# Kernel optimization log

Hardware: AMD Instinct MI355X
Metric: run time of the kernel (lower is better)

## Reference

```python
import jax, jax.numpy as jnp
import numpy as np

D = 1024      # embed_dim
H = 16        # num_heads
HD = D // H   # head_dim


def setup_inputs() -> dict:
    key = jax.random.key(0)
    ks = jax.random.split(key, 9)
    s = 0.02
    x = jax.random.normal(ks[0], (8, 1024, D), dtype=jnp.float32)
    # Per-head Q/K/V linears, torch Linear layout [out, in] -> stacked [H, HD, D]
    Wq = jax.random.normal(ks[1], (H, HD, D), dtype=jnp.float32) * s
    Wk = jax.random.normal(ks[2], (H, HD, D), dtype=jnp.float32) * s
    Wv = jax.random.normal(ks[3], (H, HD, D), dtype=jnp.float32) * s
    bq = jax.random.normal(ks[4], (H, HD), dtype=jnp.float32) * s
    bk = jax.random.normal(ks[5], (H, HD), dtype=jnp.float32) * s
    bv = jax.random.normal(ks[6], (H, HD), dtype=jnp.float32) * s
    Wo = jax.random.normal(ks[7], (D, D), dtype=jnp.float32) * s
    bo = jax.random.normal(ks[8], (D,), dtype=jnp.float32) * s
    return {"x": x, "Wq": Wq, "Wk": Wk, "Wv": Wv,
            "bq": bq, "bk": bk, "bv": bv, "Wo": Wo, "bo": bo}


def reference(x, Wq, Wk, Wv, bq, bk, bv, Wo, bo):
    # Batched per-head projections: [B,S,D] x [H,HD,D] -> [B,H,S,HD]
    q = jnp.einsum('bsd,hkd->bhsk', x, Wq) + bq[None, :, None, :]
    k = jnp.einsum('bsd,hkd->bhsk', x, Wk) + bk[None, :, None, :]
    v = jnp.einsum('bsd,hkd->bhsk', x, Wv) + bv[None, :, None, :]
    scores = jnp.einsum('bhqk,bhsk->bhqs', q, k) / jnp.sqrt(jnp.float32(HD))
    probs = jax.nn.softmax(scores, axis=-1)          # [B,H,S,S]
    attn = jnp.einsum('bhqs,bhsk->bhqk', probs, v)   # [B,H,S,HD]
    # Concat heads along feature dim -> [B,S,D]
    B, _, S, _ = attn.shape
    concat = jnp.transpose(attn, (0, 2, 1, 3)).reshape(B, S, D)
    out = jnp.einsum('bsd,ed->bse', concat, Wo) + bo  # output projection
    return out
```

## Files before the change

kernel.cpp:

```cpp
#include <hip/hip_runtime.h>
#include <stdint.h>
#include <stddef.h>


typedef short bf16x8 __attribute__((ext_vector_type(8)));
typedef float f32x4  __attribute__((ext_vector_type(4)));
typedef unsigned short u16x8 __attribute__((ext_vector_type(8)));
typedef unsigned short u16x4 __attribute__((ext_vector_type(4)));

#define MFMA16 __builtin_amdgcn_mfma_f32_16x16x32_bf16

typedef const void __attribute__((address_space(1)))* gas1_t;
typedef void __attribute__((address_space(3)))* las3_t;

static __device__ __forceinline__ void gload16(const void* g, void* l) {
  __builtin_amdgcn_global_load_lds((gas1_t)g, (las3_t)l, 16, 0, 0);
}

static __device__ __forceinline__ unsigned short f2bf(float f) {
  union { float f; unsigned int u; } v; v.f = f;
  unsigned int r = v.u + 0x7fffu + ((v.u >> 16) & 1u);
  return (unsigned short)(r >> 16);
}

__global__ __launch_bounds__(256) void cast_all(
    const float* __restrict__ x, const float* __restrict__ Wq,
    const float* __restrict__ Wk, const float* __restrict__ Wv,
    const float* __restrict__ Wo,
    unsigned short* __restrict__ xb, unsigned short* __restrict__ wqkv,
    unsigned short* __restrict__ wob) {
  int base = (blockIdx.x * 256 + threadIdx.x) * 4;
  const float* s; unsigned short* d;
  if (base < 8388608) { s = x + base; d = xb + base; }
  else if (base < 11534336) {
    int o = base - 8388608; int wi = o >> 20;
    const float* w = (wi == 0) ? Wq : (wi == 1) ? Wk : Wv;
    s = w + (o & 1048575); d = wqkv + o;
  } else {
    int o = base - 11534336; s = Wo + o; d = wob + o;
  }
  float4 f = *(const float4*)s;
  u16x4 r; r[0] = f2bf(f.x); r[1] = f2bf(f.y); r[2] = f2bf(f.z); r[3] = f2bf(f.w);
  *(u16x4*)d = r;
}

__global__ __launch_bounds__(512, 2) void gemm256_qkv(
    const unsigned short* __restrict__ Ag, const unsigned short* __restrict__ Bg,
    unsigned short* __restrict__ Qo, unsigned short* __restrict__ Ko,
    unsigned short* __restrict__ Vo,
    const float* __restrict__ bq, const float* __restrict__ bk,
    const float* __restrict__ bv) {
  __shared__ __align__(16) char sm[131072];
  const int tid = threadIdx.x, lane = tid & 63, w = tid >> 6;
  const int wr = w >> 2, wc = w & 3;
  const int l15 = lane & 15, g = lane >> 4;
  const int bcol = blockIdx.x * 256, brow = blockIdx.y * 256;

  auto stage2 = [&](int kt, int buf, int p) {
#pragma unroll
    for (int jj = 0; jj < 2; ++jj) {
      int rowBase, region;
      const unsigned short* src;
      if (p < 2) {
        int j = p * 2 + jj;
        rowBase = wr * 128 + wc * 32 + j * 8;
        region = 0; src = Ag + (size_t)(brow + rowBase) * 1024;
      } else {
        int j = (p - 2) * 2 + jj;
        rowBase = (wc >> 1) * 128 + (wr * 2 + (wc & 1)) * 32 + j * 8;
        region = 32768; src = Bg + (size_t)(bcol + rowBase) * 1024;
      }
      int rlo = lane >> 3;
      int cl = (lane & 7) ^ ((rowBase + rlo) & 7);
      gload16(src + (size_t)rlo * 1024 + kt * 64 + cl * 8,
              sm + buf * 65536 + region + rowBase * 128);
    }
  };

#pragma unroll
  for (int p = 0; p < 4; ++p) stage2(0, 0, p);
  asm volatile("s_waitcnt vmcnt(0)" ::: "memory");
  __builtin_amdgcn_s_barrier();

  f32x4 acc[8][4] = {};
  bf16x8 bfr[4];
  for (int t = 0; t < 16; ++t) {
    const int cur = t & 1;
    const char* As = sm + cur * 65536;
    const char* Bs = As + 32768;
#pragma unroll
    for (int ph = 0; ph < 4; ++ph) {
      const int qm = ph & 1, kk = ph >> 1;
      if (qm == 0) {
#pragma unroll
        for (int nc = 0; nc < 4; ++nc) {
          int row = wc * 64 + nc * 16 + l15;
          int off = (row * 128 + kk * 64 + g * 16) ^ ((row & 7) << 4);
          bfr[nc] = *(const bf16x8*)(Bs + off);
        }
      }
      bf16x8 af[4];
#pragma unroll
      for (int mr = 0; mr < 4; ++mr) {
        int row = wr * 128 + qm * 64 + mr * 16 + l15;
        int off = (row * 128 + kk * 64 + g * 16) ^ ((row & 7) << 4);
        af[mr] = *(const bf16x8*)(As + off);
      }
      if (t < 15) stage2(t + 1, cur ^ 1, ph);
      __builtin_amdgcn_s_barrier();
      __builtin_amdgcn_s_setprio(1);
#pragma unroll
      for (int mr = 0; mr < 4; ++mr)
#pragma unroll
        for (int nc = 0; nc < 4; ++nc)
          acc[qm * 4 + mr][nc] = MFMA16(af[mr], bfr[nc], acc[qm * 4 + mr][nc], 0, 0, 0);
      __builtin_amdgcn_s_setprio(0);
      if (ph == 3)
        asm volatile("s_waitcnt vmcnt(0)" ::: "memory");
      __builtin_amdgcn_s_barrier();
    }
  }

  const int bb_ = brow >> 10;
#pragma unroll
  for (int nc = 0; nc < 4; ++nc) {
    int n = bcol + wc * 64 + nc * 16 + l15;
    int tt = n >> 10, nh = n & 1023;
    int h = nh >> 6, hd = nh & 63;
    const float* bias = (tt == 0) ? bq : (tt == 1) ? bk : bv;
    float bbv = bias[nh];
    if (tt == 2) {
      size_t vtb = ((size_t)(bb_ * 16 + h) * 64 + hd) * 1024;
#pragma unroll
      for (int qm = 0; qm < 2; ++qm)
#pragma unroll
        for (int mr = 0; mr < 4; ++mr) {
          int m0 = brow + wr * 128 + qm * 64 + mr * 16 + g * 4;
          int srow0 = m0 & 1023;
          u16x4 vv;
#pragma unroll
          for (int r = 0; r < 4; ++r) vv[r] = f2bf(acc[qm * 4 + mr][nc][r] + bbv);
          *(u16x4*)(Vo + vtb + srow0) = vv;
        }
    } else {
      float scale = (tt == 0) ? 0.125f : 1.0f;
      unsigned short* dst = (tt == 0) ? Qo : Ko;
      size_t basei = ((size_t)(bb_ * 16 + h) * 1024) * 64 + hd;
#pragma unroll
      for (int qm = 0; qm < 2; ++qm)
#pragma unroll
        for (int mr = 0; mr < 4; ++mr)
#pragma unroll
          for (int r = 0; r < 4; ++r) {
            int m = brow + wr * 128 + qm * 64 + mr * 16 + g * 4 + r;
            dst[basei + (size_t)(m & 1023) * 64] = f2bf((acc[qm * 4 + mr][nc][r] + bbv) * scale);
          }
    }
  }
}

__global__ __launch_bounds__(256) void gemm128_out(
    const unsigned short* __restrict__ A, const unsigned short* __restrict__ Bm,
    float* __restrict__ Cf, const float* __restrict__ bO) {
  __shared__ __align__(16) char sm[65536];
  const int tid = threadIdx.x, lane = tid & 63, w = tid >> 6;
  const int wr = w >> 1, wc = w & 1;
  const int bcol = (blockIdx.x & 7) * 128, brow = (blockIdx.x >> 3) * 128;
  const int l15 = lane & 15, g = lane >> 4;

  auto stage = [&](int ks, int buf) {
    char* Ad = sm + buf * 32768;
    char* Bd = Ad + 16384;
#pragma unroll
    for (int jj = 0; jj < 4; ++jj) {
      int p = (w * 4 + jj) * 1024 + lane * 16;
      int row = p >> 7;
      int cl = (lane & 7) ^ (row & 7);
      gload16(A + (size_t)(brow + row) * 1024 + ks * 64 + cl * 8,
              Ad + (w * 4 + jj) * 1024);
      gload16(Bm + (size_t)(bcol + row) * 1024 + ks * 64 + cl * 8,
              Bd + (w * 4 + jj) * 1024);
    }
  };

  stage(0, 0);
  asm volatile("s_waitcnt vmcnt(0)" ::: "memory");
  __syncthreads();

  f32x4 acc[4][4] = {};
  for (int ks = 0; ks < 16; ++ks) {
    const int cur = ks & 1;
    if (ks < 15) stage(ks + 1, cur ^ 1);
    const char* As = sm + cur * 32768;
    const char* Bs = As + 16384;
#pragma unroll
    for (int kk = 0; kk < 2; ++kk) {
      bf16x8 af[4], bfr[4];
#pragma unroll
      for (int mi = 0; mi < 4; ++mi) {
        int row = wr * 64 + mi * 16 + l15;
        int off = (row * 128 + kk * 64 + g * 16) ^ ((row & 7) << 4);
        af[mi] = *(const bf16x8*)(As + off);
      }
#pragma unroll
      for (int ni = 0; ni < 4; ++ni) {
        int row = wc * 64 + ni * 16 + l15;
        int off = (row * 128 + kk * 64 + g * 16) ^ ((row & 7) << 4);
        bfr[ni] = *(const bf16x8*)(Bs + off);
      }
#pragma unroll
      for (int mi = 0; mi < 4; ++mi)
#pragma unroll
        for (int ni = 0; ni < 4; ++ni)
          acc[mi][ni] = MFMA16(af[mi], bfr[ni], acc[mi][ni], 0, 0, 0);
    }
    asm volatile("s_waitcnt vmcnt(0)" ::: "memory");
    __syncthreads();
  }
#pragma unroll
  for (int ni = 0; ni < 4; ++ni) {
    int n = bcol + wc * 64 + ni * 16 + l15;
    float bb = bO[n];
#pragma unroll
    for (int mi = 0; mi < 4; ++mi)
#pragma unroll
      for (int r = 0; r < 4; ++r) {
        int m = brow + wr * 64 + mi * 16 + g * 4 + r;
        Cf[(size_t)m * 1024 + n] = acc[mi][ni][r] + bb;
      }
  }
}

__global__ __launch_bounds__(256, 3) void attn_fused(
    const unsigned short* __restrict__ Qb, const unsigned short* __restrict__ Kb,
    const unsigned short* __restrict__ VtG, unsigned short* __restrict__ Cc) {
  __shared__ __align__(16) char sm[49152];
  char* Ks = sm;
  char* Vt = sm + 16384;
  const int tid = threadIdx.x, lane = tid & 63, w = tid >> 6;
  char* Ps = sm + 32768 + w * 4096;
  const int l15 = lane & 15, g = lane >> 4;
  const int id = blockIdx.x;
  const int qt = id >> 7, bh = id & 127;
  const size_t hb = (size_t)bh * (1024 * 64);

  bf16x8 qreg[2][2];
#pragma unroll
  for (int kk = 0; kk < 2; ++kk)
#pragma unroll
    for (int ni = 0; ni < 2; ++ni) {
      int q = qt * 128 + w * 32 + ni * 16 + l15;
      qreg[kk][ni] = *(const bf16x8*)(Qb + hb + (size_t)q * 64 + kk * 32 + g * 8);
    }

  auto stage = [&](int c, int buf) {
#pragma unroll
    for (int j = 0; j < 2; ++j) {
      int p = (w * 2 + j) * 1024 + lane * 16;
      int row = p >> 7;
      int cl = (lane & 7) ^ (row & 7);
      gload16(Kb + hb + (size_t)(c * 64 + row) * 64 + cl * 8,
              Ks + buf * 8192 + (w * 2 + j) * 1024);
      gload16(VtG + hb + (size_t)row * 1024 + c * 64 + cl * 8,
              Vt + buf * 8192 + (w * 2 + j) * 1024);
    }
  };

  stage(0, 0);
  asm volatile("s_waitcnt vmcnt(0)" ::: "memory");
  __syncthreads();

  f32x4 acc[4][2] = {};
  float m_run[2] = {-1e30f, -1e30f};
  float l_run[2] = {0.f, 0.f};

  for (int c = 0; c < 16; ++c) {
    const int cur = c & 1;
    if (c < 15) stage(c + 1, cur ^ 1);
    const char* Kc = Ks + cur * 8192;
    const char* Vc = Vt + cur * 8192;

    f32x4 st[4][2] = {};
#pragma unroll
    for (int kk = 0; kk < 2; ++kk) {
      bf16x8 ka[4];
#pragma unroll
      for (int mi = 0; mi < 4; ++mi) {
        int row = mi * 16 + l15;
        int off = (row * 128 + kk * 64 + g * 16) ^ ((row & 7) << 4);
        ka[mi] = *(const bf16x8*)(Kc + off);
      }
#pragma unroll
      for (int mi = 0; mi < 4; ++mi)
#pragma unroll
        for (int ni = 0; ni < 2; ++ni)
          st[mi][ni] = MFMA16(ka[mi], qreg[kk][ni], st[mi][ni], 0, 0, 0);
    }

    float corr_s[2];
#pragma unroll
    for (int ni = 0; ni < 2; ++ni) {
      float mx = -1e30f;
#pragma unroll
      for (int mi = 0; mi < 4; ++mi)
#pragma unroll
        for (int r = 0; r < 4; ++r) mx = fmaxf(mx, st[mi][ni][r]);
      mx = fmaxf(mx, __shfl_xor(mx, 16));
      mx = fmaxf(mx, __shfl_xor(mx, 32));
      float mn = fmaxf(m_run[ni], mx);
      float corr = __expf(m_run[ni] - mn);
      float sum = 0.f;
      const int q = ni * 16 + l15;
      const int rbase = q * 128, sw = (q & 7) << 4;
#pragma unroll
      for (int mi = 0; mi < 4; ++mi) {
        u16x4 pk;
#pragma unroll
        for (int r = 0; r < 4; ++r) {
          float e = __expf(st[mi][ni][r] - mn);
          sum += e;
          pk[r] = f2bf(e);
        }
        *(u16x4*)(Ps + ((rbase + (mi * 16 + g * 4) * 2) ^ sw)) = pk;
      }
      sum += __shfl_xor(sum, 16);
      sum += __shfl_xor(sum, 32);
      l_run[ni] = l_run[ni] * corr + sum;
      m_run[ni] = mn;
      corr_s[ni] = corr;
    }

#pragma unroll
    for (int nd = 0; nd < 4; ++nd)
#pragma unroll
      for (int ni = 0; ni < 2; ++ni)
#pragma unroll
        for (int r = 0; r < 4; ++r)
          acc[nd][ni][r] *= corr_s[ni];

#pragma unroll
    for (int kk = 0; kk < 2; ++kk) {
      bf16x8 vf[4], pa[2];
#pragma unroll
      for (int nd = 0; nd < 4; ++nd) {
        int row = nd * 16 + l15;
        int off = (row * 128 + kk * 64 + g * 16) ^ ((row & 7) << 4);
        vf[nd] = *(const bf16x8*)(Vc + off);
      }
#pragma unroll
      for (int ni = 0; ni < 2; ++ni) {
        int q = ni * 16 + l15;
        int off = (q * 128 + kk * 64 + g * 16) ^ ((q & 7) << 4);
        pa[ni] = *(const bf16x8*)(Ps + off);
      }
#pragma unroll
      for (int nd = 0; nd < 4; ++nd)
#pragma unroll
        for (int ni = 0; ni < 2; ++ni)
          acc[nd][ni] = MFMA16(vf[nd], pa[ni], acc[nd][ni], 0, 0, 0);
    }

    asm volatile("s_waitcnt vmcnt(0)" ::: "memory");
    __syncthreads();
  }

  const int b = bh >> 4, h = bh & 15;
  float invl[2] = {1.f / l_run[0], 1.f / l_run[1]};
#pragma unroll
  for (int ni = 0; ni < 2; ++ni) {
    int q = qt * 128 + w * 32 + ni * 16 + l15;
    size_t rowb = (size_t)(b * 1024 + q) * 1024 + h * 64;
#pragma unroll
    for (int nd = 0; nd < 4; ++nd) {
      u16x4 o;
#pragma unroll
      for (int r = 0; r < 4; ++r) o[r] = f2bf(acc[nd][ni][r] * invl[ni]);
      *(u16x4*)(Cc + rowb + nd * 16 + g * 4) = o;
    }
  }
}

extern "C" void kernel_launch(void* const* d_in, const int* in_sizes, int n_in,
                              void* d_out, int out_size, void* d_ws, size_t ws_size,
                              hipStream_t stream) {
  const float* x  = (const float*)d_in[0];
  const float* Wq = (const float*)d_in[1];
  const float* Wk = (const float*)d_in[2];
  const float* Wv = (const float*)d_in[3];
  const float* bq = (const float*)d_in[4];
  const float* bk = (const float*)d_in[5];
  const float* bv = (const float*)d_in[6];
  const float* Wo = (const float*)d_in[7];
  const float* bo = (const float*)d_in[8];

  char* ws = (char*)d_ws;
  unsigned short* xb   = (unsigned short*)(ws);
  unsigned short* wqkv = (unsigned short*)(ws + 16777216);
  unsigned short* wob  = (unsigned short*)(ws + 23068672);
  unsigned short* Qb   = (unsigned short*)(ws + 25165824);
  unsigned short* Kb   = (unsigned short*)(ws + 41943040);
  unsigned short* VtG  = (unsigned short*)(ws + 58720256);
  unsigned short* Cc   = xb;

  cast_all<<<dim3(12288), dim3(256), 0, stream>>>(x, Wq, Wk, Wv, Wo, xb, wqkv, wob);
  gemm256_qkv<<<dim3(12, 32), dim3(512), 0, stream>>>(
      xb, wqkv, Qb, Kb, VtG, bq, bk, bv);
  attn_fused<<<dim3(1024), dim3(256), 0, stream>>>(Qb, Kb, VtG, Cc);
  gemm128_out<<<dim3(512), dim3(256), 0, stream>>>(Cc, wob, (float*)d_out, bo);
}
```

Baseline: 261.7 us.

## Deepen QKV GEMM pipeline to three in-flight half-K stages with new swizzle

The QKV projection GEMM now splits each 64-wide K tile into two 32-wide halves stored in separate LDS sub-buffers. Loads are issued three halves ahead, using counted vmcnt waits instead of draining to zero every tile. The LDS layout changes to 64-byte rows with a rotate-style swizzle, and B fragments are reloaded once per half. This is meant to hide global-load latency better, at the cost of more barriers per tile and finer-grained, more error-prone wait accounting.

```diff
diff --git a/kernel.cpp b/kernel.cpp
--- a/kernel.cpp
+++ b/kernel.cpp
@@ -56,67 +56,79 @@
   const int l15 = lane & 15, g = lane >> 4;
   const int bcol = blockIdx.x * 256, brow = blockIdx.y * 256;
 
-  auto stage2 = [&](int kt, int buf, int p) {
+  const int srow = (lane >> 2);
+  const int sc = lane & 3;
+  auto stageA = [&](int hh) {
+    char* Ad = sm + ((hh >> 1) & 1) * 65536 + (hh & 1) * 16384;
 #pragma unroll
     for (int jj = 0; jj < 2; ++jj) {
-      int rowBase, region;
-      const unsigned short* src;
-      if (p < 2) {
-        int j = p * 2 + jj;
-        rowBase = wr * 128 + wc * 32 + j * 8;
-        region = 0; src = Ag + (size_t)(brow + rowBase) * 1024;
-      } else {
-        int j = (p - 2) * 2 + jj;
-        rowBase = (wc >> 1) * 128 + (wr * 2 + (wc & 1)) * 32 + j * 8;
-        region = 32768; src = Bg + (size_t)(bcol + rowBase) * 1024;
-      }
-      int rlo = lane >> 3;
-      int cl = (lane & 7) ^ ((rowBase + rlo) & 7);
-      gload16(src + (size_t)rlo * 1024 + kt * 64 + cl * 8,
-              sm + buf * 65536 + region + rowBase * 128);
+      int r0 = (w * 2 + jj) * 16;
+      int r = r0 + srow;
+      int gph = (sc - (r >> 1)) & 3;
+      gload16(Ag + (size_t)(brow + r) * 1024 + hh * 32 + gph * 8, Ad + r0 * 64);
     }
   };
-
-#pragma unroll
-  for (int p = 0; p < 4; ++p) stage2(0, 0, p);
-  asm volatile("s_waitcnt vmcnt(0)" ::: "memory");
+  auto stageB = [&](int hh) {
+    char* Bd = sm + ((hh >> 1) & 1) * 65536 + 32768 + (hh & 1) * 16384;
+#pragma unroll
+    for (int jj = 0; jj < 2; ++jj) {
+      int r0 = (w * 2 + jj) * 16;
+      int r = r0 + srow;
+      int gph = (sc - (r >> 1)) & 3;
+      gload16(Bg + (size_t)(bcol + r) * 1024 + hh * 32 + gph * 8, Bd + r0 * 64);
+    }
+  };
+
+  stageA(0); stageB(0); stageA(1); stageB(1); stageA(2); stageB(2);
+  asm volatile("s_waitcnt vmcnt(8)" ::: "memory");
   __builtin_amdgcn_s_barrier();
 
   f32x4 acc[8][4] = {};
-  bf16x8 bfr[4];
   for (int t = 0; t < 16; ++t) {
-    const int cur = t & 1;
-    const char* As = sm + cur * 65536;
-    const char* Bs = As + 32768;
-#pragma unroll
-    for (int ph = 0; ph < 4; ++ph) {
-      const int qm = ph & 1, kk = ph >> 1;
-      if (qm == 0) {
-#pragma unroll
-        for (int nc = 0; nc < 4; ++nc) {
-          int row = wc * 64 + nc * 16 + l15;
-          int off = (row * 128 + kk * 64 + g * 16) ^ ((row & 7) << 4);
-          bfr[nc] = *(const bf16x8*)(Bs + off);
-        }
-      }
-      bf16x8 af[4];
+    const char* Tb = sm + (t & 1) * 65536;
+#pragma unroll
+    for (int kk = 0; kk < 2; ++kk) {
+      const int h = t * 2 + kk;
+      const char* Ab = Tb + kk * 16384;
+      const char* Bb = Tb + 32768 + kk * 16384;
+      bf16x8 bfr[4], af[4];
+#pragma unroll
+      for (int nc = 0; nc < 4; ++nc) {
+        int nr = wc * 64 + nc * 16 + l15;
+        bfr[nc] = *(const bf16x8*)(Bb + nr * 64 + (((g + (nr >> 1)) & 3) << 4));
+      }
 #pragma unroll
       for (int mr = 0; mr < 4; ++mr) {
-        int row = wr * 128 + qm * 64 + mr * 16 + l15;
-        int off = (row * 128 + kk * 64 + g * 16) ^ ((row & 7) << 4);
-        af[mr] = *(const bf16x8*)(As + off);
-      }
-      if (t < 15) stage2(t + 1, cur ^ 1, ph);
+        int m = wr * 128 + mr * 16 + l15;
+        af[mr] = *(const bf16x8*)(Ab + m * 64 + (((g + (m >> 1)) & 3) << 4));
+      }
+      if (h < 29) stageA(h + 3);
       __builtin_amdgcn_s_barrier();
       __builtin_amdgcn_s_setprio(1);
 #pragma unroll
       for (int mr = 0; mr < 4; ++mr)
 #pragma unroll
         for (int nc = 0; nc < 4; ++nc)
-          acc[qm * 4 + mr][nc] = MFMA16(af[mr], bfr[nc], acc[qm * 4 + mr][nc], 0, 0, 0);
+          acc[mr][nc] = MFMA16(af[mr], bfr[nc], acc[mr][nc], 0, 0, 0);
       __builtin_amdgcn_s_setprio(0);
-      if (ph == 3)
-        asm volatile("s_waitcnt vmcnt(0)" ::: "memory");
+      __builtin_amdgcn_s_barrier();
+#pragma unroll
+      for (int mr = 0; mr < 4; ++mr) {
+        int m = wr * 128 + 64 + mr * 16 + l15;
+        af[mr] = *(const bf16x8*)(Ab + m * 64 + (((g + (m >> 1)) & 3) << 4));
+      }
+      if (h < 29) stageB(h + 3);
+      __builtin_amdgcn_s_barrier();
+      __builtin_amdgcn_s_setprio(1);
+#pragma unroll
+      for (int mr = 0; mr < 4; ++mr)
+#pragma unroll
+        for (int nc = 0; nc < 4; ++nc)
+          acc[4 + mr][nc] = MFMA16(af[mr], bfr[nc], acc[4 + mr][nc], 0, 0, 0);
+      __builtin_amdgcn_s_setprio(0);
+      if (h < 29)      asm volatile("s_waitcnt vmcnt(8)" ::: "memory");
+      else if (h == 29) asm volatile("s_waitcnt vmcnt(4)" ::: "memory");
+      else              asm volatile("s_waitcnt vmcnt(0)" ::: "memory");
       __builtin_amdgcn_s_barrier();
     }
   }
@@ -136,11 +148,10 @@
 #pragma unroll
         for (int mr = 0; mr < 4; ++mr) {
           int m0 = brow + wr * 128 + qm * 64 + mr * 16 + g * 4;
-          int srow0 = m0 & 1023;
           u16x4 vv;
 #pragma unroll
           for (int r = 0; r < 4; ++r) vv[r] = f2bf(acc[qm * 4 + mr][nc][r] + bbv);
-          *(u16x4*)(Vo + vtb + srow0) = vv;
+          *(u16x4*)(Vo + vtb + (m0 & 1023)) = vv;
         }
     } else {
       float scale = (tt == 0) ? 0.125f : 1.0f;
```

Measured after the change: 262.2 us. Within noise of the previous version (+0.2%).
